# Kernel tuning notes

Measured on AMD Instinct MI355X. Metric: run time of the kernel, lower is better.

The kernel has to match this reference:

```python
import jax, jax.numpy as jnp
import numpy as np

BETA = 0.25
B, D, H, W = 32, 64, 32, 32
K = 1024


def setup_inputs() -> dict:
    key = jax.random.key(0)
    k1, k2 = jax.random.split(key)
    z = jax.random.normal(k1, (B, D, H, W), dtype=jnp.float32)
    embedding = jax.random.normal(k2, (K, D), dtype=jnp.float32)
    return {"z": z, "embedding": embedding}


def reference(z, embedding):
    # NCHW -> NHWC, flatten to [N, D]
    zp = jnp.transpose(z, (0, 2, 3, 1))          # [B,H,W,D]
    zf = zp.reshape(-1, zp.shape[-1])            # [N,D]
    # squared-distance matrix: ||z||^2 + ||e||^2 - 2 z e^T  -> [N,K]
    d = (jnp.sum(zf * zf, axis=1, keepdims=True)
         + jnp.sum(embedding * embedding, axis=1)
         - 2.0 * (zf @ embedding.T))
    min_encoding_indices = jnp.argmin(d, axis=1)  # [N]
    z_q = embedding[min_encoding_indices].reshape(zp.shape)  # [B,H,W,D]
    # commitment / codebook losses
    e_latent_loss = jnp.mean((jax.lax.stop_gradient(z_q) - zp) ** 2)
    q_latent_loss = jnp.mean((z_q - jax.lax.stop_gradient(zp)) ** 2)
    loss = q_latent_loss + BETA * e_latent_loss
    # straight-through estimator
    z_q_st = zp + jax.lax.stop_gradient(z_q - zp)
    z_q_out = jnp.transpose(z_q_st, (0, 3, 1, 2))  # back to NCHW
    return (z_q_out, min_encoding_indices, loss)
```

## Files before the change

### kernel.cpp

```cpp
#include <hip/hip_runtime.h>


#define IDX_OFF 2097152
#define LOSS_OFF 2129920
#define BIGF 160.0f
#define RL 72
#define U32INF 0xFFFFFFFFu

typedef __attribute__((ext_vector_type(8))) _Float16 f16x8;
typedef __attribute__((ext_vector_type(4))) float f32x4;

__device__ __align__(256) float g_ep[1024 * RL];
__device__ __align__(256) float g_enb[1024];
__device__ __align__(256) unsigned short g_bf[64 * 2 * 64 * 8];
__device__ float g_partial[512];

typedef const __attribute__((address_space(1))) void* gvp;
typedef __attribute__((address_space(3))) void* lvp;

__device__ __forceinline__ void gll16(const void* g, void* l) {
    __builtin_amdgcn_global_load_lds((gvp)g, (lvp)l, 16, 0, 0);
}

__device__ __forceinline__ unsigned int min16u(unsigned int x) {
#pragma unroll
    for (int o = 1; o < 16; o <<= 1) {
        unsigned int y = __shfl_xor((int)x, o, 64);
        x = y < x ? y : x;
    }
    return x;
}

__global__ __launch_bounds__(256) void vq_prep(const float* __restrict__ e) {
    int lane = threadIdx.x & 63;
    int k    = blockIdx.x * 4 + (threadIdx.x >> 6);
    float v  = e[k * 64 + lane];
    float m2 = -2.0f * v;
    float s  = v * v;
#pragma unroll
    for (int o = 32; o; o >>= 1) s += __shfl_xor(s, o, 64);
    g_ep[(size_t)k * RL + lane] = m2;
    if (lane == 0) { g_ep[(size_t)k * RL + 64] = s + BIGF; g_enb[k] = s + BIGF; }
    _Float16 h = (_Float16)m2;
    unsigned short hb = *(unsigned short*)&h;
    int g  = k >> 4, c = k & 15;
    int ch = lane >> 5, dc = lane & 31;
    int g4 = dc >> 3,  j = dc & 7;
    int l  = g4 * 16 + c;
    g_bf[(size_t)((g * 2 + ch) * 64 + l) * 8 + j] = hb;
}

__global__ __launch_bounds__(256, 2) void vq_main(const float* __restrict__ z,
                                                  const float* __restrict__ e,
                                                  float* __restrict__ out) {
    __shared__ unsigned short bf[2][8 * 1024];
    __shared__ float enb[1024];
    __shared__ int   stop[64][3];
    __shared__ unsigned long long skey[3][64];
    __shared__ int   ishare[64];
    __shared__ float lred[4];

    const int t    = threadIdx.x;
    const int lane = t & 63;
    const int w    = __builtin_amdgcn_readfirstlane(t >> 6);
    const int col  = lane & 15;
    const int g4   = lane >> 4;
    const int bid  = blockIdx.x;
    const int b    = bid >> 4;
    const int hw0  = (bid & 15) << 6;

    gll16((const char*)g_enb + w * 1024 + lane * 16, (char*)enb + w * 1024);
#pragma unroll
    for (int i = 0; i < 4; ++i) {
        int seg = w * 4 + i;
        gll16((const char*)g_bf + seg * 1024 + lane * 16,
              (char*)&bf[0][0] + seg * 1024);
    }

    const float* zr = z + (size_t)b * 65536 + hw0 + (w * 16 + col);
    f16x8 zh[2];
#pragma unroll
    for (int c = 0; c < 2; ++c)
#pragma unroll
        for (int j = 0; j < 8; ++j) {
            int d = c * 32 + g4 * 8 + j;
            zh[c][j] = (_Float16)zr[(size_t)d * 1024];
        }

    unsigned int t0[4], t1[4], t2[4];
#pragma unroll
    for (int r = 0; r < 4; ++r) { t0[r] = U32INF; t1[r] = U32INF; t2[r] = U32INF; }

    __syncthreads();

    for (int tt = 0; tt < 8; ++tt) {
        const int cur = tt & 1;
        if (tt < 7) {
#pragma unroll
            for (int i = 0; i < 4; ++i) {
                int seg = w * 4 + i;
                gll16((const char*)g_bf + (tt + 1) * 16384 + seg * 1024 + lane * 16,
                      (char*)&bf[cur ^ 1][0] + seg * 1024);
            }
        }

        const unsigned short* bfc = &bf[cur][0];
#pragma unroll
        for (int gg = 0; gg < 8; ++gg) {
            const int kc = (tt * 8 + gg) * 16 + col;
            const f16x8* p = (const f16x8*)(bfc + gg * 1024);
            f16x8 eh0 = p[0 * 64 + lane];
            f16x8 eh1 = p[1 * 64 + lane];

            f32x4 acc = {0.f, 0.f, 0.f, 0.f};
            acc = __builtin_amdgcn_mfma_f32_16x16x32_f16(zh[0], eh0, acc, 0, 0, 0);
            acc = __builtin_amdgcn_mfma_f32_16x16x32_f16(zh[1], eh1, acc, 0, 0, 0);

            float enbv = enb[kc];
#pragma unroll
            for (int r = 0; r < 4; ++r) {
                float cand = acc[r] + enbv;
                unsigned int key = (__float_as_uint(cand) & 0xFFFFFC00u) | (unsigned)kc;
                unsigned int a0 = t0[r] < key ? t0[r] : key;
                unsigned int x  = t0[r] < key ? key : t0[r];
                unsigned int a1 = t1[r] < x ? t1[r] : x;
                unsigned int y  = t1[r] < x ? x : t1[r];
                unsigned int a2 = t2[r] < y ? t2[r] : y;
                t0[r] = a0; t1[r] = a1; t2[r] = a2;
            }
        }
        __syncthreads();
    }

#pragma unroll
    for (int r = 0; r < 4; ++r) {
        unsigned int x = t0[r], y = t1[r], zz = t2[r];
        unsigned int m1 = min16u(x);
        if (x == m1) { x = y; y = zz; zz = U32INF; }
        unsigned int m2 = min16u(x);
        if (x == m2) { x = y; }
        unsigned int m3 = min16u(x);
        int row = w * 16 + g4 * 4 + r;
        if (col == 0) {
            stop[row][0] = (int)(m1 & 1023u);
            stop[row][1] = (int)(m2 & 1023u);
            stop[row][2] = (int)(m3 & 1023u);
        }
    }
    __syncthreads();

    if (w < 3) {
        int kc = stop[lane][w];
        const float* zbase = z + (size_t)b * 65536 + hw0 + lane;
        const float* ep    = g_ep + (size_t)kc * RL;
        float d0 = 0.f, d1 = 0.f, d2 = 0.f, d3 = 0.f;
#pragma unroll
        for (int dq = 0; dq < 16; ++dq) {
            float4 ev = *(const float4*)(ep + dq * 4);
            d0 = fmaf(zbase[(size_t)(dq * 4 + 0) * 1024], ev.x, d0);
            d1 = fmaf(zbase[(size_t)(dq * 4 + 1) * 1024], ev.y, d1);
            d2 = fmaf(zbase[(size_t)(dq * 4 + 2) * 1024], ev.z, d2);
            d3 = fmaf(zbase[(size_t)(dq * 4 + 3) * 1024], ev.w, d3);
        }
        float dist = (d0 + d1) + (d2 + d3) + ep[64];
        skey[w][lane] = ((unsigned long long)__float_as_uint(dist) << 32) | (unsigned)kc;
    }
    __syncthreads();

    if (w == 0) {
        unsigned long long ky = skey[0][lane];
        unsigned long long k1 = skey[1][lane];
        unsigned long long k2 = skey[2][lane];
        ky = k1 < ky ? k1 : ky;
        ky = k2 < ky ? k2 : ky;
        int idx = (int)(ky & 0xFFFFFFFFull);
        out[IDX_OFF + bid * 64 + lane] = (float)idx;
        ishare[lane] = idx;
    }
    __syncthreads();

    {
        int idx = ishare[lane];
        const float*  zbase = z + (size_t)b * 65536 + hw0 + lane;
        float*        qbase = out + (size_t)b * 65536 + hw0 + lane;
        const float4* er4   = (const float4*)(e + (size_t)idx * 64) + (w << 2);

        float lsum = 0.f;
#pragma unroll
        for (int p = 0; p < 4; ++p) {
            float4 ev = er4[p];
            int d = (w << 4) + (p << 2);
            float ezw[4] = {ev.x, ev.y, ev.z, ev.w};
#pragma unroll
            for (int qq = 0; qq < 4; ++qq) {
                float zv = zbase[(size_t)(d + qq) * 1024];
                float df = ezw[qq] - zv;
                lsum = fmaf(df, df, lsum);
                qbase[(size_t)(d + qq) * 1024] = ezw[qq];
            }
        }
#pragma unroll
        for (int o = 32; o; o >>= 1) lsum += __shfl_xor(lsum, o, 64);
        if (lane == 0) lred[w] = lsum;
    }
    __syncthreads();
    if (t == 0)
        g_partial[bid] = (lred[0] + lred[1]) + (lred[2] + lred[3]);
}

__global__ __launch_bounds__(64) void vq_finish(float* __restrict__ out) {
    int lane = threadIdx.x;
    float s = 0.f;
#pragma unroll
    for (int i = 0; i < 8; ++i) s += g_partial[lane * 8 + i];
#pragma unroll
    for (int o = 32; o; o >>= 1) s += __shfl_xor(s, o, 64);
    if (lane == 0) out[LOSS_OFF] = s * (1.25f / 2097152.0f);
}

extern "C" void kernel_launch(void* const* d_in, const int* in_sizes, int n_in,
                              void* d_out, int out_size, void* d_ws, size_t ws_size,
                              hipStream_t stream) {
    const float* z = (const float*)d_in[0];
    const float* e = (const float*)d_in[1];
    float* out = (float*)d_out;

    vq_prep<<<256, 256, 0, stream>>>(e);
    vq_main<<<512, 256, 0, stream>>>(z, e, out);
    vq_finish<<<1, 64, 0, stream>>>(out);
}
```

Before: 29.95 us.

## Quad-buffer codebook tiles, drop g_ep table, and fold loss finish into main kernel

The main kernel now prefetches codebook fp16 tiles two steps ahead into four LDS buffers. It uses explicit vmcnt waits and a single s_barrier per step instead of a double buffer with two syncthreads. The z loads are issued first and drained before the async LDS loads, so the vmcnt accounting stays correct. The precomputed -2e table is removed, and exact rescoring reads the embedding directly and uses enb from LDS. The separate finish kernel is replaced by a last-block atomic counter reduction, which saves a launch. LDS per block grows, which may reduce occupancy at 2 blocks per CU.

After: 42.39 us. 41.5% more time.

```diff
diff --git a/kernel.cpp b/kernel.cpp
--- a/kernel.cpp
+++ b/kernel.cpp
@@ -4,16 +4,15 @@
 #define IDX_OFF 2097152
 #define LOSS_OFF 2129920
 #define BIGF 160.0f
-#define RL 72
 #define U32INF 0xFFFFFFFFu
 
 typedef __attribute__((ext_vector_type(8))) _Float16 f16x8;
 typedef __attribute__((ext_vector_type(4))) float f32x4;
 
-__device__ __align__(256) float g_ep[1024 * RL];
 __device__ __align__(256) float g_enb[1024];
 __device__ __align__(256) unsigned short g_bf[64 * 2 * 64 * 8];
 __device__ float g_partial[512];
+__device__ unsigned g_done;
 
 typedef const __attribute__((address_space(1))) void* gvp;
 typedef __attribute__((address_space(3))) void* lvp;
@@ -39,8 +38,8 @@
     float s  = v * v;
 #pragma unroll
     for (int o = 32; o; o >>= 1) s += __shfl_xor(s, o, 64);
-    g_ep[(size_t)k * RL + lane] = m2;
-    if (lane == 0) { g_ep[(size_t)k * RL + 64] = s + BIGF; g_enb[k] = s + BIGF; }
+    if (lane == 0) g_enb[k] = s + BIGF;
+    if (blockIdx.x == 0 && threadIdx.x == 0) g_done = 0u;
     _Float16 h = (_Float16)m2;
     unsigned short hb = *(unsigned short*)&h;
     int g  = k >> 4, c = k & 15;
@@ -53,12 +52,13 @@
 __global__ __launch_bounds__(256, 2) void vq_main(const float* __restrict__ z,
                                                   const float* __restrict__ e,
                                                   float* __restrict__ out) {
-    __shared__ unsigned short bf[2][8 * 1024];
+    __shared__ unsigned short bf[4][8 * 1024];
     __shared__ float enb[1024];
     __shared__ int   stop[64][3];
     __shared__ unsigned long long skey[3][64];
     __shared__ int   ishare[64];
     __shared__ float lred[4];
+    __shared__ unsigned lastFlag;
 
     const int t    = threadIdx.x;
     const int lane = t & 63;
@@ -69,6 +69,18 @@
     const int b    = bid >> 4;
     const int hw0  = (bid & 15) << 6;
 
+    const float* zr = z + (size_t)b * 65536 + hw0 + (w * 16 + col);
+    f16x8 zh[2];
+#pragma unroll
+    for (int c = 0; c < 2; ++c)
+#pragma unroll
+        for (int j = 0; j < 8; ++j) {
+            int d = c * 32 + g4 * 8 + j;
+            zh[c][j] = (_Float16)zr[(size_t)d * 1024];
+        }
+    asm volatile("s_waitcnt vmcnt(0)" ::: "memory");
+    __builtin_amdgcn_sched_barrier(0);
+
     gll16((const char*)g_enb + w * 1024 + lane * 16, (char*)enb + w * 1024);
 #pragma unroll
     for (int i = 0; i < 4; ++i) {
@@ -76,35 +88,36 @@
         gll16((const char*)g_bf + seg * 1024 + lane * 16,
               (char*)&bf[0][0] + seg * 1024);
     }
-
-    const float* zr = z + (size_t)b * 65536 + hw0 + (w * 16 + col);
-    f16x8 zh[2];
-#pragma unroll
-    for (int c = 0; c < 2; ++c)
-#pragma unroll
-        for (int j = 0; j < 8; ++j) {
-            int d = c * 32 + g4 * 8 + j;
-            zh[c][j] = (_Float16)zr[(size_t)d * 1024];
-        }
+#pragma unroll
+    for (int i = 0; i < 4; ++i) {
+        int seg = w * 4 + i;
+        gll16((const char*)g_bf + 16384 + seg * 1024 + lane * 16,
+              (char*)&bf[1][0] + seg * 1024);
+    }
 
     unsigned int t0[4], t1[4], t2[4];
 #pragma unroll
     for (int r = 0; r < 4; ++r) { t0[r] = U32INF; t1[r] = U32INF; t2[r] = U32INF; }
 
-    __syncthreads();
-
     for (int tt = 0; tt < 8; ++tt) {
-        const int cur = tt & 1;
-        if (tt < 7) {
+        if (tt < 6) {
 #pragma unroll
             for (int i = 0; i < 4; ++i) {
                 int seg = w * 4 + i;
-                gll16((const char*)g_bf + (tt + 1) * 16384 + seg * 1024 + lane * 16,
-                      (char*)&bf[cur ^ 1][0] + seg * 1024);
+                gll16((const char*)g_bf + (tt + 2) * 16384 + seg * 1024 + lane * 16,
+                      (char*)&bf[(tt + 2) & 3][0] + seg * 1024);
             }
-        }
-
-        const unsigned short* bfc = &bf[cur][0];
+            asm volatile("s_waitcnt vmcnt(8)" ::: "memory");
+        } else if (tt == 6) {
+            asm volatile("s_waitcnt vmcnt(4)" ::: "memory");
+        } else {
+            asm volatile("s_waitcnt vmcnt(0)" ::: "memory");
+        }
+        __builtin_amdgcn_sched_barrier(0);
+        __builtin_amdgcn_s_barrier();
+        __builtin_amdgcn_sched_barrier(0);
+
+        const unsigned short* bfc = &bf[tt & 3][0];
 #pragma unroll
         for (int gg = 0; gg < 8; ++gg) {
             const int kc = (tt * 8 + gg) * 16 + col;
@@ -129,7 +142,6 @@
                 t0[r] = a0; t1[r] = a1; t2[r] = a2;
             }
         }
-        __syncthreads();
     }
 
 #pragma unroll
@@ -152,7 +164,7 @@
     if (w < 3) {
         int kc = stop[lane][w];
         const float* zbase = z + (size_t)b * 65536 + hw0 + lane;
-        const float* ep    = g_ep + (size_t)kc * RL;
+        const float* ep    = e + (size_t)kc * 64;
         float d0 = 0.f, d1 = 0.f, d2 = 0.f, d3 = 0.f;
 #pragma unroll
         for (int dq = 0; dq < 16; ++dq) {
@@ -162,7 +174,7 @@
             d2 = fmaf(zbase[(size_t)(dq * 4 + 2) * 1024], ev.z, d2);
             d3 = fmaf(zbase[(size_t)(dq * 4 + 3) * 1024], ev.w, d3);
         }
-        float dist = (d0 + d1) + (d2 + d3) + ep[64];
+        float dist = fmaf(-2.0f, (d0 + d1) + (d2 + d3), enb[kc]);
         skey[w][lane] = ((unsigned long long)__float_as_uint(dist) << 32) | (unsigned)kc;
     }
     __syncthreads();
@@ -204,18 +216,22 @@
         if (lane == 0) lred[w] = lsum;
     }
     __syncthreads();
-    if (t == 0)
+
+    if (t == 0) {
         g_partial[bid] = (lred[0] + lred[1]) + (lred[2] + lred[3]);
-}
-
-__global__ __launch_bounds__(64) void vq_finish(float* __restrict__ out) {
-    int lane = threadIdx.x;
-    float s = 0.f;
-#pragma unroll
-    for (int i = 0; i < 8; ++i) s += g_partial[lane * 8 + i];
-#pragma unroll
-    for (int o = 32; o; o >>= 1) s += __shfl_xor(s, o, 64);
-    if (lane == 0) out[LOSS_OFF] = s * (1.25f / 2097152.0f);
+        __threadfence();
+        lastFlag = (atomicAdd(&g_done, 1u) == 511u);
+    }
+    __syncthreads();
+    if (lastFlag && w == 0) {
+        __threadfence();
+        float s = 0.f;
+#pragma unroll
+        for (int i = 0; i < 8; ++i) s += g_partial[lane * 8 + i];
+#pragma unroll
+        for (int o = 32; o; o >>= 1) s += __shfl_xor(s, o, 64);
+        if (lane == 0) out[LOSS_OFF] = s * (1.25f / 2097152.0f);
+    }
 }
 
 extern "C" void kernel_launch(void* const* d_in, const int* in_sizes, int n_in,
@@ -227,5 +243,4 @@
 
     vq_prep<<<256, 256, 0, stream>>>(e);
     vq_main<<<512, 256, 0, stream>>>(z, e, out);
-    vq_finish<<<1, 64, 0, stream>>>(out);
-}
+}
```
